# Kernel tuning notes

Measured on AMD Instinct MI355X. Metric: run time of the kernel, lower is better.

## Reference

```python
import jax, jax.numpy as jnp
import numpy as np

N = 100000          # nodes
E = 1600000         # edges
D_IN = 128
HID = 256
N_CLASSES = 10
N_GRAPHS = 64


def gcn_conv(x, src, dst, W, b, n_nodes):
    """PyG GCNConv: add self-loops, symmetric deg^{-1/2} normalization, x@W, scatter-add."""
    h = x @ W  # [N, out]
    loop = jnp.arange(n_nodes, dtype=src.dtype)
    src2 = jnp.concatenate([src, loop])
    dst2 = jnp.concatenate([dst, loop])
    deg = jax.ops.segment_sum(jnp.ones(src2.shape[0], x.dtype), dst2, num_segments=n_nodes)
    dinv = jax.lax.rsqrt(deg)  # deg >= 1 thanks to self-loops
    norm = dinv[src2] * dinv[dst2]  # [E+N]
    msg = norm[:, None] * h[src2]   # [E+N, out]
    return jax.ops.segment_sum(msg, dst2, num_segments=n_nodes) + b


def setup_inputs() -> dict:
    key = jax.random.key(0)
    ks = jax.random.split(key, 12)
    x = jax.random.normal(ks[0], (N, D_IN), dtype=jnp.float32)
    edge_index = jax.random.randint(ks[1], (2, E), 0, N, dtype=jnp.int64)
    batch = jnp.sort(jax.random.randint(ks[2], (N,), 0, N_GRAPHS, dtype=jnp.int64))
    def glorot(k, shape):
        lim = float(np.sqrt(6.0 / (shape[0] + shape[1])))
        return jax.random.uniform(k, shape, jnp.float32, -lim, lim)
    W1 = glorot(ks[3], (D_IN, HID));  b1 = jnp.zeros((HID,), jnp.float32)
    W2 = glorot(ks[4], (HID, HID));   b2 = jnp.zeros((HID,), jnp.float32)
    Wf1 = glorot(ks[5], (HID, HID));  bf1 = jnp.zeros((HID,), jnp.float32)
    Wf2 = glorot(ks[6], (HID, N_CLASSES)); bf2 = jnp.zeros((N_CLASSES,), jnp.float32)
    return {"x": x, "edge_index": edge_index, "batch": batch,
            "W1": W1, "b1": b1, "W2": W2, "b2": b2,
            "Wf1": Wf1, "bf1": bf1, "Wf2": Wf2, "bf2": bf2}


def reference(x, edge_index, batch, W1, b1, W2, b2, Wf1, bf1, Wf2, bf2):
    src, dst = edge_index[0], edge_index[1]
    h = jax.nn.relu(gcn_conv(x, src, dst, W1, b1, N))
    h = jax.nn.relu(gcn_conv(h, src, dst, W2, b2, N))
    # global mean pool over graph ids
    summed = jax.ops.segment_sum(h, batch, num_segments=N_GRAPHS)  # [G, HID]
    counts = jax.ops.segment_sum(jnp.ones((N,), h.dtype), batch, num_segments=N_GRAPHS)
    pooled = summed / jnp.maximum(counts, 1.0)[:, None]
    z = jax.nn.relu(pooled @ Wf1 + bf1)
    alpha = jax.nn.softplus(z @ Wf2 + bf2) + 0.001
    return alpha
```

## Files before the change

kernel.cpp:

```cpp
#include <hip/hip_runtime.h>
#include <math.h>

#define NN   100000
#define NE   1600000
#define DIN  128
#define HID  256
#define NG   64
#define NCLS 10

#define NBLK 128
#define EPB  (NE / NBLK)
#define NBUK 512
#define NPB  196
#define NHIST (NBUK * NBLK)

using bf16x8 = __attribute__((ext_vector_type(8))) short;
using f32x4  = __attribute__((ext_vector_type(4))) float;
using f32x2  = __attribute__((ext_vector_type(2))) float;
using u32x2  = __attribute__((ext_vector_type(2))) unsigned int;

static __device__ __forceinline__ unsigned short f2bf(float f) {
    unsigned u = __float_as_uint(f);
    u += 0x7fff + ((u >> 16) & 1);
    return (unsigned short)(u >> 16);
}

static __device__ __forceinline__ unsigned char f32_to_fp8(float f) {
    float a = fminf(fabsf(f), 448.f);
    unsigned bits = __float_as_uint(a * 0x1p-120f);
    bits += 0x7ffff + ((bits >> 20) & 1);
    unsigned e4 = (bits >> 20) & 0x7f;
    return (unsigned char)(e4 | (f < 0.f ? 0x80u : 0u));
}
#if __has_builtin(__builtin_amdgcn_cvt_pk_f32_fp8)
#define HAVE_CVT_FP8 1
#endif
static __device__ __forceinline__ void fp8x4_to_f32(unsigned u, float* f) {
#ifdef HAVE_CVT_FP8
    f32x2 lo = __builtin_amdgcn_cvt_pk_f32_fp8((int)u, false);
    f32x2 hi = __builtin_amdgcn_cvt_pk_f32_fp8((int)u, true);
    f[0] = lo[0]; f[1] = lo[1]; f[2] = hi[0]; f[3] = hi[1];
#else
#pragma unroll
    for (int k = 0; k < 4; ++k) {
        unsigned b = (u >> (8 * k)) & 0xffu;
        unsigned bits = ((b & 0x80u) << 24) | ((b & 0x7fu) << 20);
        f[k] = __uint_as_float(bits) * 0x1p+120f;
    }
#endif
}
static __device__ __forceinline__ int4 fp8x8_to_bf16x8(unsigned lo, unsigned hi) {
    float f[8];
    fp8x4_to_f32(lo, f);
    fp8x4_to_f32(hi, f + 4);
    int4 r;
    r.x = (int)((__float_as_uint(f[0]) >> 16) | (__float_as_uint(f[1]) & 0xffff0000u));
    r.y = (int)((__float_as_uint(f[2]) >> 16) | (__float_as_uint(f[3]) & 0xffff0000u));
    r.z = (int)((__float_as_uint(f[4]) >> 16) | (__float_as_uint(f[5]) & 0xffff0000u));
    r.w = (int)((__float_as_uint(f[6]) >> 16) | (__float_as_uint(f[7]) & 0xffff0000u));
    return r;
}


__global__ __launch_bounds__(256) void k_hist(const int* __restrict__ dst,
                                              int* __restrict__ histg) {
    __shared__ int h[NBUK];
    const int t = threadIdx.x;
    for (int i = t; i < NBUK; i += 256) h[i] = 0;
    __syncthreads();
    const int e0 = blockIdx.x * EPB, e1 = e0 + EPB;
    for (int e = e0 + t; e < e1; e += 256)
        atomicAdd(&h[(unsigned)__builtin_nontemporal_load(&dst[e]) / NPB], 1);
    __syncthreads();
    for (int i = t; i < NBUK; i += 256)
        histg[i * NBLK + blockIdx.x] = h[i];
}

__global__ __launch_bounds__(256) void k_bsum2(const int* __restrict__ d,
                                               int* __restrict__ bsum) {
    __shared__ int sd[256];
    int t = threadIdx.x;
    const int4 v = *(const int4*)&d[blockIdx.x * 1024 + t * 4];
    sd[t] = v.x + v.y + v.z + v.w;
    __syncthreads();
    for (int off = 128; off > 0; off >>= 1) {
        if (t < off) sd[t] += sd[t + off];
        __syncthreads();
    }
    if (t == 0) bsum[blockIdx.x] = sd[0];
}

__global__ void k_scanb2(const int* __restrict__ bsum, int* __restrict__ boff,
                         const int* __restrict__ batch, float* __restrict__ countsf) {
    __shared__ int tmp[64];
    int t = threadIdx.x;
    int v = bsum[t];
    tmp[t] = v; __syncthreads();
    for (int off = 1; off < 64; off <<= 1) {
        int u = (t >= off) ? tmp[t - off] : 0;
        __syncthreads();
        tmp[t] += u;
        __syncthreads();
    }
    boff[t] = tmp[t] - v;
    int g = t;
    int lo = 0, hi = NN;
    while (lo < hi) { int mid = (lo + hi) >> 1; if (batch[mid] < g) lo = mid + 1; else hi = mid; }
    int lb = lo;
    lo = 0; hi = NN;
    while (lo < hi) { int mid = (lo + hi) >> 1; if (batch[mid] <= g) lo = mid + 1; else hi = mid; }
    countsf[g] = (float)(lo - lb);
}

__global__ __launch_bounds__(256) void k_offs2(int* __restrict__ d,
                                               const int* __restrict__ boff) {
    __shared__ int ts[256];
    int t = threadIdx.x;
    int base = blockIdx.x * 1024 + t * 4;
    int4 v = *(const int4*)&d[base];
    int s = v.x + v.y + v.z + v.w;
    ts[t] = s; __syncthreads();
    for (int off = 1; off < 256; off <<= 1) {
        int u = (t >= off) ? ts[t - off] : 0;
        __syncthreads();
        ts[t] += u;
        __syncthreads();
    }
    int run = ts[t] - s + boff[blockIdx.x];
    int4 o;
    o.x = run; run += v.x;
    o.y = run; run += v.y;
    o.z = run; run += v.z;
    o.w = run; run += v.w;
    *(int4*)&d[base] = o;
}

__global__ __launch_bounds__(256) void k_scatter(const int* __restrict__ src,
                                                 const int* __restrict__ dst,
                                                 const int* __restrict__ offg,
                                                 unsigned* __restrict__ pairs) {
    __shared__ int cur[NBUK];
    const int t = threadIdx.x;
    for (int i = t; i < NBUK; i += 256) cur[i] = offg[i * NBLK + blockIdx.x];
    __syncthreads();
    const int e0 = blockIdx.x * EPB, e1 = e0 + EPB;
    for (int e = e0 + t; e < e1; e += 256) {
        int d = __builtin_nontemporal_load(&dst[e]);
        int sv = __builtin_nontemporal_load(&src[e]);
        int b = (unsigned)d / NPB;
        int li = d - b * NPB;
        unsigned pk = ((unsigned)li << 24) | (unsigned)sv;
        int p = atomicAdd(&cur[b], 1);
        __builtin_nontemporal_store(pk, &pairs[p]);
    }
}

__global__ __launch_bounds__(256) void k_csr(const unsigned* __restrict__ pairs,
                                             const int* __restrict__ offg,
                                             int* __restrict__ csr,
                                             int* __restrict__ deg,
                                             float* __restrict__ dinv,
                                             int* __restrict__ offs) {
    __shared__ int cnt[NPB];
    __shared__ int loff[256];
    __shared__ int cur[NPB];
    const int b = blockIdx.x, t = threadIdx.x;
    const int s     = offg[b * NBLK];
    const int e_end = (b == NBUK - 1) ? NE : offg[(b + 1) * NBLK];
    const int nb0   = b * NPB;
    const int nnod  = min(NPB, NN - nb0);
    if (t < NPB) cnt[t] = 0;
    __syncthreads();
    for (int e = s + t; e < e_end; e += 256)
        atomicAdd(&cnt[pairs[e] >> 24], 1);
    __syncthreads();
    int v = (t < NPB) ? cnt[t] : 0;
    loff[t] = v;
    __syncthreads();
    for (int off = 1; off < 256; off <<= 1) {
        int u = (t >= off) ? loff[t - off] : 0;
        __syncthreads();
        loff[t] += u;
        __syncthreads();
    }
    int myoff = loff[t] - v;
    __syncthreads();
    loff[t] = myoff;
    if (t < NPB) cur[t] = 0;
    __syncthreads();
    if (t < nnod) {
        int node = nb0 + t;
        int dg = cnt[t];
        deg[node]  = dg;
        dinv[node] = rsqrtf((float)(dg + 1));
        offs[node] = s + myoff;
    }
    for (int e = s + t; e < e_end; e += 256) {
        unsigned pk = pairs[e];
        int li = pk >> 24;
        int p = atomicAdd(&cur[li], 1);
        csr[s + loff[li] + p] = (int)(pk & 0xffffffu);
    }
}


#define XQ (NN * 32)

__global__ void k_cast_all(const float* __restrict__ x, const float* __restrict__ dinv,
                           unsigned char* __restrict__ xs8,
                           const float* __restrict__ W1, unsigned short* __restrict__ Wt1,
                           const float* __restrict__ W2, unsigned short* __restrict__ Wt2) {
    int i = blockIdx.x * blockDim.x + threadIdx.x;
    if (i < XQ) {
        int nd = i >> 5;
        int q  = i & 31;
        float dv = dinv[nd];
        const float4 v = *(const float4*)&x[(size_t)nd * DIN + q * 4];
        uchar4 o;
        o.x = f32_to_fp8(v.x * dv); o.y = f32_to_fp8(v.y * dv);
        o.z = f32_to_fp8(v.z * dv); o.w = f32_to_fp8(v.w * dv);
        *(uchar4*)&xs8[(size_t)nd * DIN + q * 4] = o;
        return;
    }
    int j = i - XQ;
    if (j < DIN * HID) {
        int k = j >> 8, nc = j & 255;
        Wt1[nc * DIN + k] = f2bf(W1[j]);
    } else if (j < (DIN + HID) * HID) {
        int jj = j - DIN * HID;
        int k = jj >> 8, nc = jj & 255;
        Wt2[nc * HID + k] = f2bf(W2[jj]);
    }
}


template <int MODE>
__global__ __launch_bounds__(256) void k_gemm_mfma(const unsigned char* __restrict__ A8,
                                                   const unsigned short* __restrict__ Wt,
                                                   const float* __restrict__ dinv,
                                                   const float* __restrict__ bias,
                                                   void* __restrict__ outp,
                                                   const int* __restrict__ batch,
                                                   float* __restrict__ pooled,
                                                   int M, int K) {
    __shared__ unsigned short As[128 * 40];
    __shared__ unsigned short Bs[128 * 40];
    __shared__ float psum[4][128];
    __shared__ int gloc[128];
    const int t = threadIdx.x;
    const int lane = t & 63;
    const int wid = t >> 6;
    const int wr = wid >> 1, wc = wid & 1;
    const int bm = blockIdx.x * 128, bn = blockIdx.y * 128;
    const int lr = lane & 15;
    const int ko = (lane >> 4) << 3;

    f32x4 acc[4][4] = {};

    const int r = t >> 2;
    const int kq = (t & 3) << 3;

    int g0 = 0;
    if (MODE == 2) {
        g0 = batch[bm];
        for (int i = t; i < 4 * 128; i += 256) ((float*)psum)[i] = 0.f;
        if (t < 128) gloc[t] = (bm + t < M) ? (batch[bm + t] - g0) : 0;
    }

    for (int kk = 0; kk < K; kk += 32) {
#pragma unroll
        for (int h = 0; h < 128; h += 64) {
            int row = bm + r + h;
            int4 o = make_int4(0, 0, 0, 0);
            if (row < M) {
                u32x2 v = *(const u32x2*)&A8[(size_t)row * K + kk + kq];
                o = fp8x8_to_bf16x8(v.x, v.y);
            }
            *(int4*)&As[(r + h) * 40 + kq] = o;
        }
#pragma unroll
        for (int h = 0; h < 128; h += 64) {
            int nrow = bn + r + h;
            int4 v = *(const int4*)&Wt[(size_t)nrow * K + kk + kq];
            *(int4*)&Bs[(r + h) * 40 + kq] = v;
        }
        __syncthreads();
        bf16x8 af[4], bfr[4];
#pragma unroll
        for (int mf = 0; mf < 4; ++mf)
            af[mf] = *(const bf16x8*)&As[(wr * 64 + mf * 16 + lr) * 40 + ko];
#pragma unroll
        for (int nf = 0; nf < 4; ++nf)
            bfr[nf] = *(const bf16x8*)&Bs[(wc * 64 + nf * 16 + lr) * 40 + ko];
#pragma unroll
        for (int mf = 0; mf < 4; ++mf)
#pragma unroll
            for (int nf = 0; nf < 4; ++nf)
                acc[mf][nf] = __builtin_amdgcn_mfma_f32_16x16x32_bf16(af[mf], bfr[nf], acc[mf][nf], 0, 0, 0);
        __syncthreads();
    }

    if (MODE == 1) {
        unsigned char* out8 = (unsigned char*)outp;
#pragma unroll
        for (int mf = 0; mf < 4; ++mf) {
#pragma unroll
            for (int b = 0; b < 4; ++b) {
                int row = bm + wr * 64 + mf * 16 + (lane >> 4) * 4 + b;
                if (row >= M) continue;
                float dv = dinv[row];
#pragma unroll
                for (int nf = 0; nf < 4; ++nf) {
                    int col = bn + wc * 64 + nf * 16 + lr;
                    float v = fmaxf(acc[mf][nf][b] + bias[col], 0.f);
                    out8[(size_t)row * HID + col] = f32_to_fp8(dv * v);
                }
            }
        }
    } else {
        const int q4 = (lane >> 4) << 2;
#pragma unroll
        for (int nf = 0; nf < 4; ++nf) {
            const int lcol = wc * 64 + nf * 16 + lr;
            const float bb = bias[bn + lcol];
            float run = 0.f; int gcur = 0;
#pragma unroll
            for (int mf = 0; mf < 4; ++mf) {
#pragma unroll
                for (int b = 0; b < 4; ++b) {
                    int lrow = wr * 64 + mf * 16 + q4 + b;
                    if (bm + lrow < M) {
                        int gl = gloc[lrow];
                        float v = fmaxf(acc[mf][nf][b] + bb, 0.f);
                        if (gl != gcur) {
                            if (run != 0.f) {
                                if (gcur < 4) atomicAdd(&psum[gcur][lcol], run);
                                else atomicAdd(&pooled[(size_t)(g0 + gcur) * HID + bn + lcol], run);
                            }
                            run = 0.f; gcur = gl;
                        }
                        run += v;
                    }
                }
            }
            if (run != 0.f) {
                if (gcur < 4) atomicAdd(&psum[gcur][lcol], run);
                else atomicAdd(&pooled[(size_t)(g0 + gcur) * HID + bn + lcol], run);
            }
        }
        __syncthreads();
        for (int i = t; i < 4 * 128; i += 256) {
            int gl = i >> 7, lcol = i & 127;
            int g = g0 + gl;
            float v = psum[gl][lcol];
            if (g < NG && v != 0.f)
                atomicAdd(&pooled[(size_t)g * HID + bn + lcol], v);
        }
    }
}


__global__ __launch_bounds__(256) void k_agg256(const unsigned char* __restrict__ hs,
                                                const int* __restrict__ csr,
                                                const int* __restrict__ offs,
                                                const int* __restrict__ deg,
                                                const float* __restrict__ dinv,
                                                unsigned char* __restrict__ out, int n) {
    int wid = threadIdx.x >> 6, lane = threadIdx.x & 63;
    int node = blockIdx.x * 4 + wid;
    if (node >= n) return;
    int c = lane << 2;
    float a0, a1, a2, a3;
    {
        unsigned u = *(const unsigned*)&hs[(size_t)node * HID + c];
        float f[4]; fp8x4_to_f32(u, f);
        a0 = f[0]; a1 = f[1]; a2 = f[2]; a3 = f[3];
    }
    int s0 = offs[node], cnt = deg[node];
    for (int base = 0; base < cnt; base += 64) {
        int nb = min(64, cnt - base);
        int idx = (lane < nb) ? __builtin_nontemporal_load(&csr[s0 + base + lane]) : 0;
        int i = 0;
        for (; i + 8 <= nb; i += 8) {
            unsigned v[8];
#pragma unroll
            for (int k = 0; k < 8; ++k) {
                int j = __shfl(idx, i + k);
                v[k] = *(const unsigned*)&hs[(size_t)j * HID + c];
            }
#pragma unroll
            for (int k = 0; k < 8; ++k) {
                float f[4]; fp8x4_to_f32(v[k], f);
                a0 += f[0]; a1 += f[1]; a2 += f[2]; a3 += f[3];
            }
        }
        for (; i + 4 <= nb; i += 4) {
            unsigned v[4];
#pragma unroll
            for (int k = 0; k < 4; ++k) {
                int j = __shfl(idx, i + k);
                v[k] = *(const unsigned*)&hs[(size_t)j * HID + c];
            }
#pragma unroll
            for (int k = 0; k < 4; ++k) {
                float f[4]; fp8x4_to_f32(v[k], f);
                a0 += f[0]; a1 += f[1]; a2 += f[2]; a3 += f[3];
            }
        }
        for (; i < nb; ++i) {
            int j = __shfl(idx, i);
            unsigned u = *(const unsigned*)&hs[(size_t)j * HID + c];
            float f[4]; fp8x4_to_f32(u, f);
            a0 += f[0]; a1 += f[1]; a2 += f[2]; a3 += f[3];
        }
    }
    float dv = dinv[node];
    uchar4 r;
    r.x = f32_to_fp8(dv * a0); r.y = f32_to_fp8(dv * a1);
    r.z = f32_to_fp8(dv * a2); r.w = f32_to_fp8(dv * a3);
    *(uchar4*)&out[(size_t)node * HID + c] = r;
}


__global__ __launch_bounds__(256) void k_agg128(const unsigned char* __restrict__ xs,
                                                const int* __restrict__ csr,
                                                const int* __restrict__ offs,
                                                const int* __restrict__ deg,
                                                const float* __restrict__ dinv,
                                                unsigned char* __restrict__ out, int n) {
    int wid = threadIdx.x >> 6, lane = threadIdx.x & 63;
    int node = blockIdx.x * 4 + wid;
    if (node >= n) return;
    int half = lane >> 5, l32 = lane & 31;
    int c = l32 << 2;
    float a0 = 0.f, a1 = 0.f, a2 = 0.f, a3 = 0.f;
    if (half == 0) {
        unsigned u = *(const unsigned*)&xs[(size_t)node * DIN + c];
        float f[4]; fp8x4_to_f32(u, f);
        a0 = f[0]; a1 = f[1]; a2 = f[2]; a3 = f[3];
    }
    int s0 = offs[node], cnt = deg[node];
    for (int base = 0; base < cnt; base += 64) {
        int nb = min(64, cnt - base);
        int idx = (lane < nb) ? __builtin_nontemporal_load(&csr[s0 + base + lane]) : 0;
        int i = 0;
        for (; i + 8 <= nb; i += 8) {
            unsigned v[4];
#pragma unroll
            for (int k = 0; k < 4; ++k) {
                int j = __shfl(idx, i + 2 * k + half);
                v[k] = *(const unsigned*)&xs[(size_t)j * DIN + c];
            }
#pragma unroll
            for (int k = 0; k < 4; ++k) {
                float f[4]; fp8x4_to_f32(v[k], f);
                a0 += f[0]; a1 += f[1]; a2 += f[2]; a3 += f[3];
            }
        }
        for (; i < nb; i += 2) {
            int e = i + half;
            int j = __shfl(idx, e < nb ? e : 0);
            if (e < nb) {
                unsigned u = *(const unsigned*)&xs[(size_t)j * DIN + c];
                float f[4]; fp8x4_to_f32(u, f);
                a0 += f[0]; a1 += f[1]; a2 += f[2]; a3 += f[3];
            }
        }
    }
    a0 += __shfl_xor(a0, 32);
    a1 += __shfl_xor(a1, 32);
    a2 += __shfl_xor(a2, 32);
    a3 += __shfl_xor(a3, 32);
    if (half == 0) {
        float dv = dinv[node];
        uchar4 r;
        r.x = f32_to_fp8(dv * a0); r.y = f32_to_fp8(dv * a1);
        r.z = f32_to_fp8(dv * a2); r.w = f32_to_fp8(dv * a3);
        *(uchar4*)&out[(size_t)node * DIN + c] = r;
    }
}


__global__ __launch_bounds__(256) void k_mlp(const float* __restrict__ pooled,
                                             const float* __restrict__ countsf,
                                             const float* __restrict__ Wf1,
                                             const float* __restrict__ bf1,
                                             const float* __restrict__ Wf2,
                                             const float* __restrict__ bf2,
                                             float* __restrict__ out) {
    __shared__ float p[HID];
    __shared__ float z[HID];
    int g = blockIdx.x, t = threadIdx.x;
    float cnt = fmaxf(countsf[g], 1.0f);
    p[t] = pooled[g * HID + t] / cnt;
    __syncthreads();
    float accz = bf1[t];
    for (int k = 0; k < HID; ++k)
        accz = fmaf(p[k], Wf1[k * HID + t], accz);
    z[t] = fmaxf(accz, 0.f);
    __syncthreads();
    if (t < NCLS) {
        float o = bf2[t];
        for (int k = 0; k < HID; ++k)
            o = fmaf(z[k], Wf2[k * NCLS + t], o);
        float sp = fmaxf(o, 0.f) + log1pf(expf(-fabsf(o)));
        out[g * NCLS + t] = sp + 0.001f;
    }
}


extern "C" void kernel_launch(void* const* d_in, const int* in_sizes, int n_in,
                              void* d_out, int out_size, void* d_ws, size_t ws_size,
                              hipStream_t stream) {
    const float* x     = (const float*)d_in[0];
    const int*   ei    = (const int*)d_in[1];
    const int*   batch = (const int*)d_in[2];
    const float* W1    = (const float*)d_in[3];
    const float* b1    = (const float*)d_in[4];
    const float* W2    = (const float*)d_in[5];
    const float* b2    = (const float*)d_in[6];
    const float* Wf1   = (const float*)d_in[7];
    const float* bf1   = (const float*)d_in[8];
    const float* Wf2   = (const float*)d_in[9];
    const float* bf2   = (const float*)d_in[10];
    float* out = (float*)d_out;

    const int* srcv = ei;
    const int* dstv = ei + NE;

    char* p = (char*)d_ws;
    auto take = [&](size_t bytes) -> char* {
        char* q = p; p += (bytes + 255) & ~(size_t)255; return q;
    };
    char* big0 = take((size_t)NN * HID * 2);
    char* big1 = take((size_t)NN * HID * 2);
    unsigned char*  xs8 = (unsigned char*)big0;
    unsigned char*  xa8 = (unsigned char*)(big0 + (size_t)NN * DIN);
    unsigned char*  h8  = (unsigned char*)big1;
    unsigned char*  r8  = (unsigned char*)big0;
    unsigned* pairs = (unsigned*)big1;
    unsigned short* wt1  = (unsigned short*)take((size_t)DIN * HID * 2);
    unsigned short* wt2  = (unsigned short*)take((size_t)HID * HID * 2);
    int*   histg   = (int*)take((size_t)NHIST * 4);
    int*   bsum    = (int*)take(64 * 4);
    int*   boff    = (int*)take(64 * 4);
    int*   deg     = (int*)take((size_t)NN * 4);
    int*   offs    = (int*)take((size_t)NN * 4);
    int*   csr     = (int*)take((size_t)NE * 4);
    float* dinv    = (float*)take((size_t)NN * 4);
    float* pooled  = (float*)take((size_t)NG * HID * 4);
    float* countsf = (float*)take((size_t)NG * 4);

    hipMemsetAsync(pooled, 0, (size_t)NG * HID * 4, stream);

    k_hist<<<NBLK, 256, 0, stream>>>(dstv, histg);
    k_bsum2<<<64, 256, 0, stream>>>(histg, bsum);
    k_scanb2<<<1, 64, 0, stream>>>(bsum, boff, batch, countsf);
    k_offs2<<<64, 256, 0, stream>>>(histg, boff);
    k_scatter<<<NBLK, 256, 0, stream>>>(srcv, dstv, histg, pairs);
    k_csr<<<NBUK, 256, 0, stream>>>(pairs, histg, csr, deg, dinv, offs);

    int cast_total = XQ + (DIN + HID) * HID;
    k_cast_all<<<(cast_total + 255) / 256, 256, 0, stream>>>(x, dinv, xs8, W1, wt1, W2, wt2);

    dim3 gg((NN + 127) / 128, HID / 128);
    k_agg128<<<(NN + 3) / 4, 256, 0, stream>>>(xs8, csr, offs, deg, dinv, xa8, NN);
    k_gemm_mfma<1><<<gg, 256, 0, stream>>>(xa8, wt1, dinv, b1, (void*)h8, batch, pooled, NN, DIN);
    k_agg256<<<(NN + 3) / 4, 256, 0, stream>>>(h8, csr, offs, deg, dinv, r8, NN);
    k_gemm_mfma<2><<<gg, 256, 0, stream>>>(r8, wt2, dinv, b2, nullptr, batch, pooled, NN, HID);

    k_mlp<<<NG, 256, 0, stream>>>(pooled, countsf, Wf1, bf1, Wf2, bf2, out);
}
```

Baseline: 339.1 us.

## Replace global pooling atomics with per-block partials and a deterministic reduce kernel

The second GEMM epilogue no longer issues global atomicAdds into the pooled buffer. Each block writes its four per-graph partial sums to a scratch array with nontemporal stores, and a new k_reduce kernel binary-searches graph boundaries in the sorted batch array to sum the partials per graph. Blocks whose rows all belong to one graph take a fast path that reduces with wave shuffles before touching shared memory. This also removes the memset of pooled, at the cost of an extra kernel launch and the assumption that a 128-row block spans at most four graphs (group index clamped to 3).

After: 339.1 us. Within noise of the previous version (+0.0%).

```diff
diff --git a/kernel.cpp b/kernel.cpp
--- a/kernel.cpp
+++ b/kernel.cpp
@@ -13,6 +13,7 @@
 #define NBUK 512
 #define NPB  196
 #define NHIST (NBUK * NBLK)
+#define NBR  ((NN + 127) / 128)
 
 using bf16x8 = __attribute__((ext_vector_type(8))) short;
 using f32x4  = __attribute__((ext_vector_type(4))) float;
@@ -241,7 +242,6 @@
                                                    const float* __restrict__ bias,
                                                    void* __restrict__ outp,
                                                    const int* __restrict__ batch,
-                                                   float* __restrict__ pooled,
                                                    int M, int K) {
     __shared__ unsigned short As[128 * 40];
     __shared__ unsigned short Bs[128 * 40];
@@ -260,11 +260,12 @@
     const int r = t >> 2;
     const int kq = (t & 3) << 3;
 
-    int g0 = 0;
+    int g0 = 0, gend = 0;
     if (MODE == 2) {
         g0 = batch[bm];
+        gend = batch[min(bm + 127, M - 1)];
         for (int i = t; i < 4 * 128; i += 256) ((float*)psum)[i] = 0.f;
-        if (t < 128) gloc[t] = (bm + t < M) ? (batch[bm + t] - g0) : 0;
+        if (t < 128) gloc[t] = (bm + t < M) ? min(batch[bm + t] - g0, 3) : 0;
     }
 
     for (int kk = 0; kk < K; kk += 32) {
@@ -319,44 +320,77 @@
         }
     } else {
         const int q4 = (lane >> 4) << 2;
-#pragma unroll
-        for (int nf = 0; nf < 4; ++nf) {
-            const int lcol = wc * 64 + nf * 16 + lr;
-            const float bb = bias[bn + lcol];
-            float run = 0.f; int gcur = 0;
-#pragma unroll
-            for (int mf = 0; mf < 4; ++mf) {
-#pragma unroll
-                for (int b = 0; b < 4; ++b) {
-                    int lrow = wr * 64 + mf * 16 + q4 + b;
-                    if (bm + lrow < M) {
-                        int gl = gloc[lrow];
-                        float v = fmaxf(acc[mf][nf][b] + bb, 0.f);
-                        if (gl != gcur) {
-                            if (run != 0.f) {
-                                if (gcur < 4) atomicAdd(&psum[gcur][lcol], run);
-                                else atomicAdd(&pooled[(size_t)(g0 + gcur) * HID + bn + lcol], run);
+        if (gend == g0) {
+#pragma unroll
+            for (int nf = 0; nf < 4; ++nf) {
+                const int lcol = wc * 64 + nf * 16 + lr;
+                const float bb = bias[bn + lcol];
+                float rsum = 0.f;
+#pragma unroll
+                for (int mf = 0; mf < 4; ++mf)
+#pragma unroll
+                    for (int b = 0; b < 4; ++b) {
+                        int lrow = wr * 64 + mf * 16 + q4 + b;
+                        if (bm + lrow < M) rsum += fmaxf(acc[mf][nf][b] + bb, 0.f);
+                    }
+                rsum += __shfl_xor(rsum, 16);
+                rsum += __shfl_xor(rsum, 32);
+                if ((lane >> 4) == 0) atomicAdd(&psum[0][lcol], rsum);
+            }
+        } else {
+#pragma unroll
+            for (int nf = 0; nf < 4; ++nf) {
+                const int lcol = wc * 64 + nf * 16 + lr;
+                const float bb = bias[bn + lcol];
+                float run = 0.f; int gcur = 0;
+#pragma unroll
+                for (int mf = 0; mf < 4; ++mf) {
+#pragma unroll
+                    for (int b = 0; b < 4; ++b) {
+                        int lrow = wr * 64 + mf * 16 + q4 + b;
+                        if (bm + lrow < M) {
+                            int gl = gloc[lrow];
+                            float v = fmaxf(acc[mf][nf][b] + bb, 0.f);
+                            if (gl != gcur) {
+                                if (run != 0.f) atomicAdd(&psum[gcur][lcol], run);
+                                run = 0.f; gcur = gl;
                             }
-                            run = 0.f; gcur = gl;
+                            run += v;
                         }
-                        run += v;
                     }
                 }
-            }
-            if (run != 0.f) {
-                if (gcur < 4) atomicAdd(&psum[gcur][lcol], run);
-                else atomicAdd(&pooled[(size_t)(g0 + gcur) * HID + bn + lcol], run);
-            }
-        }
-        __syncthreads();
-        for (int i = t; i < 4 * 128; i += 256) {
-            int gl = i >> 7, lcol = i & 127;
-            int g = g0 + gl;
-            float v = psum[gl][lcol];
-            if (g < NG && v != 0.f)
-                atomicAdd(&pooled[(size_t)g * HID + bn + lcol], v);
-        }
-    }
+                if (run != 0.f) atomicAdd(&psum[gcur][lcol], run);
+            }
+        }
+        __syncthreads();
+        float* scratch = (float*)outp;
+        size_t base = ((size_t)blockIdx.x * 2 + blockIdx.y) * 512;
+        for (int i = t; i < 512; i += 256)
+            __builtin_nontemporal_store(((const float*)psum)[i], &scratch[base + i]);
+    }
+}
+
+
+__global__ __launch_bounds__(128) void k_reduce(const float* __restrict__ scratch,
+                                                const int* __restrict__ batch,
+                                                float* __restrict__ pooled) {
+    const int g = blockIdx.x >> 1, by = blockIdx.x & 1;
+    const int t = threadIdx.x;
+    int lo = 0, hi = NN;
+    while (lo < hi) { int mid = (lo + hi) >> 1; if (batch[mid] < g) lo = mid + 1; else hi = mid; }
+    int s = lo;
+    lo = s; hi = NN;
+    while (lo < hi) { int mid = (lo + hi) >> 1; if (batch[mid] <= g) lo = mid + 1; else hi = mid; }
+    int e = lo;
+    float sum = 0.f;
+    if (e > s) {
+        int bx0 = s >> 7, bx1 = (e - 1) >> 7;
+        for (int bx = bx0; bx <= bx1; ++bx) {
+            int gl = min(g - batch[bx << 7], 3);
+            sum += scratch[((size_t)bx * 2 + by) * 512 + gl * 128 + t];
+        }
+    }
+    pooled[g * HID + by * 128 + t] = sum;
 }
 
 
@@ -538,6 +572,7 @@
     unsigned char*  xa8 = (unsigned char*)(big0 + (size_t)NN * DIN);
     unsigned char*  h8  = (unsigned char*)big1;
     unsigned char*  r8  = (unsigned char*)big0;
+    float* scratch = (float*)(big1 + (size_t)NN * HID);
     unsigned* pairs = (unsigned*)big1;
     unsigned short* wt1  = (unsigned short*)take((size_t)DIN * HID * 2);
     unsigned short* wt2  = (unsigned short*)take((size_t)HID * HID * 2);
@@ -551,8 +586,6 @@
     float* pooled  = (float*)take((size_t)NG * HID * 4);
     float* countsf = (float*)take((size_t)NG * 4);
 
-    hipMemsetAsync(pooled, 0, (size_t)NG * HID * 4, stream);
-
     k_hist<<<NBLK, 256, 0, stream>>>(dstv, histg);
     k_bsum2<<<64, 256, 0, stream>>>(histg, bsum);
     k_scanb2<<<1, 64, 0, stream>>>(bsum, boff, batch, countsf);
@@ -563,11 +596,12 @@
     int cast_total = XQ + (DIN + HID) * HID;
     k_cast_all<<<(cast_total + 255) / 256, 256, 0, stream>>>(x, dinv, xs8, W1, wt1, W2, wt2);
 
-    dim3 gg((NN + 127) / 128, HID / 128);
+    dim3 gg(NBR, HID / 128);
     k_agg128<<<(NN + 3) / 4, 256, 0, stream>>>(xs8, csr, offs, deg, dinv, xa8, NN);
-    k_gemm_mfma<1><<<gg, 256, 0, stream>>>(xa8, wt1, dinv, b1, (void*)h8, batch, pooled, NN, DIN);
+    k_gemm_mfma<1><<<gg, 256, 0, stream>>>(xa8, wt1, dinv, b1, (void*)h8, batch, NN, DIN);
     k_agg256<<<(NN + 3) / 4, 256, 0, stream>>>(h8, csr, offs, deg, dinv, r8, NN);
-    k_gemm_mfma<2><<<gg, 256, 0, stream>>>(r8, wt2, dinv, b2, nullptr, batch, pooled, NN, HID);
+    k_gemm_mfma<2><<<gg, 256, 0, stream>>>(r8, wt2, dinv, b2, (void*)scratch, batch, NN, HID);
+    k_reduce<<<2 * NG, 128, 0, stream>>>(scratch, batch, pooled);
 
     k_mlp<<<NG, 256, 0, stream>>>(pooled, countsf, Wf1, bf1, Wf2, bf2, out);
 }
```
